# Kernel tuning notes

Hardware: AMD Instinct MI355X
Metric: run time of the kernel (lower is better)

The kernel has to match this reference:

```python
import jax, jax.numpy as jnp
import numpy as np

NUM_ENTITIES = 64
PAD, BOS, EOS = 0, 1, 2
B, S = 512, 512


def setup_inputs() -> dict:
    key = jax.random.key(0)
    k1, k2, k3 = jax.random.split(key, 3)
    emissions = jax.random.normal(k1, (B, S, NUM_ENTITIES), dtype=jnp.float32)
    entities = jax.random.randint(k2, (B, S), 0, NUM_ENTITIES)
    mask = jnp.ones((B, S), dtype=bool)
    # transitions param, initialized as in _init_transitions
    t = jax.random.uniform(k3, (NUM_ENTITIES, NUM_ENTITIES), jnp.float32, -0.1, 0.1)
    t = t.at[:, BOS].set(-10000.0)
    t = t.at[EOS, :].set(-10000.0)
    t = t.at[PAD, :].set(-10000.0)
    t = t.at[:, PAD].set(-10000.0)
    t = t.at[PAD, PAD].set(0.0)
    t = t.at[PAD, EOS].set(0.0)
    return {"emissions": emissions, "transitions": t, "entities": entities, "mask": mask}


def _crf_nll(emissions, transitions, entities, mask):
    mf = mask.astype(emissions.dtype)  # [B,S]
    # ---- gold path score (vectorized over time) ----
    first = entities[:, 0]
    last_idx = jnp.sum(mask.astype(jnp.int32), axis=1) - 1  # [B]
    last = jnp.take_along_axis(entities, last_idx[:, None], axis=1)[:, 0]
    e = jnp.take_along_axis(emissions, entities[:, :, None], axis=2)[:, :, 0]  # [B,S]
    t = transitions[entities[:, :-1], entities[:, 1:]]  # [B,S-1]
    score = (transitions[BOS, first] + e[:, 0]
             + jnp.sum((e[:, 1:] + t) * mf[:, 1:], axis=1)
             + transitions[last, EOS])  # [B]
    # ---- log partition via scan over time ----
    alpha0 = transitions[BOS][None, :] + emissions[:, 0]  # [B,E]

    def step(alpha, xs):
        em_t, m_t = xs  # [B,E], [B] bool
        # scores[b, prev, cur] = alpha[b,prev] + T[prev,cur] + em[b,cur]
        scores = alpha[:, :, None] + transitions[None, :, :] + em_t[:, None, :]
        new_alpha = jax.nn.logsumexp(scores, axis=1)  # [B,E]
        alpha = jnp.where(m_t[:, None], new_alpha, alpha)
        return alpha, None

    alpha, _ = jax.lax.scan(step, alpha0,
                            (jnp.swapaxes(emissions[:, 1:], 0, 1), mask[:, 1:].T))
    log_z = jax.nn.logsumexp(alpha + transitions[:, EOS][None, :], axis=1)  # [B]
    return -jnp.mean(score - log_z)


def reference(emissions, transitions, entities, mask):
    return _crf_nll(emissions, transitions, entities, mask)
```

## Files before the change

### kernel.cpp

```cpp
#include <hip/hip_runtime.h>

#define NE 64
#define BB 512
#define SS 512
#define TMID 256
#define NBWD (SS - 1 - TMID)
#define NCHAIN 32
#define BOS_S 1
#define EOS_S 2
#define LN2 0.69314718055994531f
#define DR 8

typedef float f32x4 __attribute__((ext_vector_type(4)));
typedef int   i32x4 __attribute__((ext_vector_type(4)));
typedef short bf16x8 __attribute__((ext_vector_type(8)));

#define WG_SCOPE __HIP_MEMORY_SCOPE_WORKGROUP

__device__ __forceinline__ float wave_sum(float v) {
#pragma unroll
    for (int off = 32; off > 0; off >>= 1)
        v += __shfl_xor(v, off, 64);
    return v;
}

__device__ __forceinline__ unsigned pack2(float lo, float hi) {
    return __builtin_amdgcn_perm(__float_as_uint(hi), __float_as_uint(lo), 0x07060302u);
}

__device__ __forceinline__ unsigned short bf16_rne(float f) {
    unsigned u = __float_as_uint(f);
    return (unsigned short)((u + 0x7fffu + ((u >> 16) & 1u)) >> 16);
}

template <bool FWD>
__device__ __forceinline__ void producer_loop(const float* embase, float (*ring)[1024],
                                              int* ready, int* cons, int p, int lane,
                                              int tmax) {
    int t = 1 + p;
    f32x4 b0[4], b1[4];
    if (t <= tmax) {
        const float* r = embase + (size_t)(FWD ? t : (SS - t)) * NE;
#pragma unroll
        for (int m = 0; m < 4; ++m) b0[m] = *(const f32x4*)(r + 16 * m);
    }
    if (t + 3 <= tmax) {
        const float* r = embase + (size_t)(FWD ? (t + 3) : (SS - t - 3)) * NE;
#pragma unroll
        for (int m = 0; m < 4; ++m) b1[m] = *(const f32x4*)(r + 16 * m);
    }
    while (t <= tmax) {
        int tn2 = t + 6;
        f32x4 nb[4];
        if (tn2 <= tmax) {
            const float* r = embase + (size_t)(FWD ? tn2 : (SS - tn2)) * NE;
#pragma unroll
            for (int m = 0; m < 4; ++m) nb[m] = *(const f32x4*)(r + 16 * m);
        }
        while (__hip_atomic_load(cons, __ATOMIC_ACQUIRE, WG_SCOPE) < t - DR)
            __builtin_amdgcn_s_sleep(1);
        int slot = t & (DR - 1);
        f32x4* dst = (f32x4*)ring[slot];
#pragma unroll
        for (int m = 0; m < 4; ++m) {
            f32x4 w;
#pragma unroll
            for (int r2 = 0; r2 < 4; ++r2) w[r2] = __expf(b0[m][r2]);
            dst[m * 64 + lane] = w;
        }
        __hip_atomic_store(&ready[slot], t, __ATOMIC_RELEASE, WG_SCOPE);
#pragma unroll
        for (int m = 0; m < 4; ++m) { b0[m] = b1[m]; b1[m] = nb[m]; }
        t += 3;
    }
}

__global__ __launch_bounds__(512, 1) void crf_fused(const float* __restrict__ em,
                                                    const float* __restrict__ T,
                                                    const int* __restrict__ ent,
                                                    float* __restrict__ out_mean) {
    const int lane = threadIdx.x & 63;
    const int wv = threadIdx.x >> 6;

    if (blockIdx.x >= NCHAIN) {
        const int b = (blockIdx.x - NCHAIN) * 8 + wv;
        const float* emb = em + (size_t)b * SS * NE;
        const int* entb = ent + b * SS;
        float sc = 0.f;
        for (int t = lane; t < SS; t += 64) {
            int et = entb[t];
            sc += emb[t * NE + et];
            sc += (t == 0) ? T[BOS_S * NE + et] : T[entb[t - 1] * NE + et];
            if (t == SS - 1) sc += T[et * NE + EOS_S];
        }
        sc = wave_sum(sc);
        if (lane == 0) atomicAdd(out_mean, -sc * (1.0f / (float)BB));
        return;
    }

    __shared__ float ringf[DR][1024];
    __shared__ float ringb[DR][1024];
    __shared__ int readyf[DR], readyb[DR];
    __shared__ int consf, consb;
    __shared__ float wbuf[1024];
    __shared__ int shiftb_s;
    __shared__ int doneb;

    if (threadIdx.x < DR) { readyf[threadIdx.x] = 0; readyb[threadIdx.x] = 0; }
    if (threadIdx.x == 0) { consf = 0; consb = 0; doneb = 0; }
    __syncthreads();

    const int g = blockIdx.x;
    const int n = lane & 15;
    const int q = lane >> 4;

    if (wv >= 2) {
        const float* embase = em + ((size_t)(g * 16 + n) * SS) * NE + 4 * q;
        if (wv <= 4)
            producer_loop<true>(embase, ringf, readyf, &consf, wv - 2, lane, TMID);
        else
            producer_loop<false>(embase, ringb, readyb, &consb, wv - 5, lane, NBWD);
        return;
    }

#define PIPE_FLAGS(RING, READY, T_, GNXT, DO_LOAD)                               \
    do {                                                                         \
        int _fprev = fnext;                                                      \
        fnext = __hip_atomic_load(&READY[((T_) + 2) & (DR - 1)],                 \
                                  __ATOMIC_RELAXED, WG_SCOPE);                   \
        if (DO_LOAD) {                                                           \
            if (__builtin_expect(_fprev != (T_) + 1, 0)) {                       \
                while (__hip_atomic_load(&READY[((T_) + 1) & (DR - 1)],          \
                                         __ATOMIC_ACQUIRE, WG_SCOPE) != (T_) + 1) {} \
            }                                                                    \
            const f32x4* _src = (const f32x4*)RING[((T_) + 1) & (DR - 1)];       \
            GNXT[0] = _src[0 * 64 + lane];                                       \
            GNXT[1] = _src[1 * 64 + lane];                                       \
            GNXT[2] = _src[2 * 64 + lane];                                       \
            GNXT[3] = _src[3 * 64 + lane];                                       \
        }                                                                        \
    } while (0)

#define CONS_STORE(CONS, T_)                                                     \
    do {                                                                         \
        asm volatile("" ::: "memory");      \
        if ((((T_) & 1) == 0) && lane == 0)                                      \
            __hip_atomic_store(&CONS, (T_), __ATOMIC_RELAXED, WG_SCOPE);         \
    } while (0)


#define STEP_F(T_, GCUR, GNXT, DO_LOAD, DO_NORM)                                 \
    do {                                                                         \
        PIPE_FLAGS(ringf, readyf, T_, GNXT, DO_LOAD);                            \
        float ds[16];                                                            \
        if (DO_NORM) {                                                           \
            unsigned u3 = (unsigned)__builtin_amdgcn_readlane(__float_as_int(d[3]), 0); \
            int kk = (int)((u3 >> 23) & 255u) - 127;                             \
            shift += kk;                                                         \
            float scale = __uint_as_float((unsigned)(127 - kk) << 23);           \
            _Pragma("unroll") for (int v = 0; v < 16; ++v) ds[v] = d[v] * scale; \
        } else {                                                                 \
            _Pragma("unroll") for (int v = 0; v < 16; ++v) ds[v] = d[v];         \
        }                                                                        \
        i32x4 bi0, bi1;                                                          \
        bi0[0] = (int)pack2(ds[0], ds[1]);   bi0[1] = (int)pack2(ds[2], ds[3]);  \
        bi0[2] = (int)pack2(ds[4], ds[5]);   bi0[3] = (int)pack2(ds[6], ds[7]);  \
        bi1[0] = (int)pack2(ds[8], ds[9]);   bi1[1] = (int)pack2(ds[10], ds[11]);\
        bi1[2] = (int)pack2(ds[12], ds[13]); bi1[3] = (int)pack2(ds[14], ds[15]);\
        bf16x8 B0 = __builtin_bit_cast(bf16x8, bi0);                             \
        bf16x8 B1 = __builtin_bit_cast(bf16x8, bi1);                             \
        _Pragma("unroll") for (int tm = 0; tm < 4; ++tm) {                       \
            f32x4 z4 = {0.f, 0.f, 0.f, 0.f};                                     \
            f32x4 acc0 = __builtin_amdgcn_mfma_f32_16x16x32_bf16(A[tm][0], B0, z4, 0, 0, 0); \
            f32x4 acc1 = __builtin_amdgcn_mfma_f32_16x16x32_bf16(A[tm][1], B1, z4, 0, 0, 0); \
            _Pragma("unroll") for (int r = 0; r < 4; ++r)                        \
                d[4 * tm + r] = (acc0[r] + acc1[r]) * GCUR[tm][r];               \
        }                                                                        \
        CONS_STORE(consf, T_);                                                   \
    } while (0)

#define STEP_B(T_, GCUR, GNXT, DO_LOAD, DO_NORM)                                 \
    do {                                                                         \
        PIPE_FLAGS(ringb, readyb, T_, GNXT, DO_LOAD);                            \
        float ds[16];                                                            \
        if (DO_NORM) {                                                           \
            unsigned u3 = (unsigned)__builtin_amdgcn_readlane(__float_as_int(d[3]), 0); \
            int kk = (int)((u3 >> 23) & 255u) - 127;                             \
            shift += kk;                                                         \
            float scale = __uint_as_float((unsigned)(127 - kk) << 23);           \
            _Pragma("unroll") for (int v = 0; v < 16; ++v)                       \
                ds[v] = (d[v] * GCUR[v >> 2][v & 3]) * scale;                    \
        } else {                                                                 \
            _Pragma("unroll") for (int v = 0; v < 16; ++v)                       \
                ds[v] = d[v] * GCUR[v >> 2][v & 3];                              \
        }                                                                        \
        i32x4 bi0, bi1;                                                          \
        bi0[0] = (int)pack2(ds[0], ds[1]);   bi0[1] = (int)pack2(ds[2], ds[3]);  \
        bi0[2] = (int)pack2(ds[4], ds[5]);   bi0[3] = (int)pack2(ds[6], ds[7]);  \
        bi1[0] = (int)pack2(ds[8], ds[9]);   bi1[1] = (int)pack2(ds[10], ds[11]);\
        bi1[2] = (int)pack2(ds[12], ds[13]); bi1[3] = (int)pack2(ds[14], ds[15]);\
        bf16x8 B0 = __builtin_bit_cast(bf16x8, bi0);                             \
        bf16x8 B1 = __builtin_bit_cast(bf16x8, bi1);                             \
        _Pragma("unroll") for (int tm = 0; tm < 4; ++tm) {                       \
            f32x4 z4 = {0.f, 0.f, 0.f, 0.f};                                     \
            f32x4 acc0 = __builtin_amdgcn_mfma_f32_16x16x32_bf16(A[tm][0], B0, z4, 0, 0, 0); \
            f32x4 acc1 = __builtin_amdgcn_mfma_f32_16x16x32_bf16(A[tm][1], B1, z4, 0, 0, 0); \
            _Pragma("unroll") for (int r = 0; r < 4; ++r)                        \
                d[4 * tm + r] = acc0[r] + acc1[r];                               \
        }                                                                        \
        CONS_STORE(consb, T_);                                                   \
    } while (0)

    if (wv == 0) {
        __builtin_amdgcn_s_setprio(1);
        const int b = g * 16 + n;

        bf16x8 A[4][2];
#pragma unroll
        for (int tm = 0; tm < 4; ++tm)
#pragma unroll
            for (int kt = 0; kt < 2; ++kt) {
                i32x4 w;
#pragma unroll
                for (int pp = 0; pp < 4; ++pp) {
                    int j0 = 2 * pp, j1 = 2 * pp + 1;
                    int s0 = 16 * (2 * kt + (j0 >> 2)) + 4 * q + (j0 & 3);
                    int s1 = 16 * (2 * kt + (j1 >> 2)) + 4 * q + (j1 & 3);
                    int m = 16 * tm + n;
                    unsigned lo = bf16_rne(__expf(T[s0 * NE + m]));
                    unsigned hi = bf16_rne(__expf(T[s1 * NE + m]));
                    w[pp] = (int)(lo | (hi << 16));
                }
                A[tm][kt] = __builtin_bit_cast(bf16x8, w);
            }

        const float* pe = em + (size_t)b * SS * NE + 4 * q;
        float d[16];
        {
            f32x4 e0[4];
#pragma unroll
            for (int m = 0; m < 4; ++m) e0[m] = *(const f32x4*)(pe + 16 * m);
#pragma unroll
            for (int v = 0; v < 16; ++v) {
                int s = 16 * (v >> 2) + 4 * q + (v & 3);
                d[v] = __expf(T[BOS_S * NE + s] + e0[v >> 2][v & 3]);
            }
        }

        int shift = 0;
        f32x4 GA[4], GB[4];
        while (__hip_atomic_load(&readyf[1], __ATOMIC_ACQUIRE, WG_SCOPE) != 1) {}
        {
            const f32x4* _src = (const f32x4*)ringf[1];
            GA[0] = _src[0 * 64 + lane]; GA[1] = _src[1 * 64 + lane];
            GA[2] = _src[2 * 64 + lane]; GA[3] = _src[3 * 64 + lane];
        }
        int fnext = __hip_atomic_load(&readyf[2], __ATOMIC_RELAXED, WG_SCOPE);

        int t = 1;
        for (; t + 4 <= TMID; t += 4) {
            STEP_F(t,     GA, GB, 1, 1);
            STEP_F(t + 1, GB, GA, 1, 0);
            STEP_F(t + 2, GA, GB, 1, 0);
            STEP_F(t + 3, GB, GA, 1, 0);
        }
        STEP_F(t,     GA, GB, 1, 1);
        STEP_F(t + 1, GB, GA, 1, 0);
        STEP_F(t + 2, GA, GB, 1, 0);
        STEP_F(t + 3, GB, GA, 0, 0);

        while (__hip_atomic_load(&doneb, __ATOMIC_ACQUIRE, WG_SCOPE) == 0) {}
        int sb = shiftb_s;
        const float* wp = wbuf + n * 64 + q * 16;
        float partial = 0.f;
#pragma unroll
        for (int v = 0; v < 16; ++v) partial = fmaf(d[v], wp[v], partial);
        partial += __shfl_xor(partial, 16, 64);
        partial += __shfl_xor(partial, 32, 64);

        float log_z = (float)(shift + sb) * LN2 + __logf(partial);
        float val = (lane < 16) ? log_z * (1.0f / (float)BB) : 0.f;
        val = wave_sum(val);
        if (lane == 0) atomicAdd(out_mean, val);
        return;
    }

    {
        __builtin_amdgcn_s_setprio(1);
        bf16x8 A[4][2];
#pragma unroll
        for (int tm = 0; tm < 4; ++tm)
#pragma unroll
            for (int kt = 0; kt < 2; ++kt) {
                i32x4 w;
#pragma unroll
                for (int pp = 0; pp < 4; ++pp) {
                    int j0 = 2 * pp, j1 = 2 * pp + 1;
                    int s0 = 16 * (2 * kt + (j0 >> 2)) + 4 * q + (j0 & 3);
                    int s1 = 16 * (2 * kt + (j1 >> 2)) + 4 * q + (j1 & 3);
                    int m = 16 * tm + n;
                    unsigned lo = bf16_rne(__expf(T[m * NE + s0]));
                    unsigned hi = bf16_rne(__expf(T[m * NE + s1]));
                    w[pp] = (int)(lo | (hi << 16));
                }
                A[tm][kt] = __builtin_bit_cast(bf16x8, w);
            }

        float d[16];
#pragma unroll
        for (int v = 0; v < 16; ++v) {
            int s = 16 * (v >> 2) + 4 * q + (v & 3);
            d[v] = __expf(T[s * NE + EOS_S]);
        }

        int shift = 0;
        f32x4 GA[4], GB[4];
        while (__hip_atomic_load(&readyb[1], __ATOMIC_ACQUIRE, WG_SCOPE) != 1) {}
        {
            const f32x4* _src = (const f32x4*)ringb[1];
            GA[0] = _src[0 * 64 + lane]; GA[1] = _src[1 * 64 + lane];
            GA[2] = _src[2 * 64 + lane]; GA[3] = _src[3 * 64 + lane];
        }
        int fnext = __hip_atomic_load(&readyb[2], __ATOMIC_RELAXED, WG_SCOPE);

        int vt = 1;
        for (; vt + 4 <= NBWD; vt += 4) {
            STEP_B(vt,     GA, GB, 1, 1);
            STEP_B(vt + 1, GB, GA, 1, 0);
            STEP_B(vt + 2, GA, GB, 1, 0);
            STEP_B(vt + 3, GB, GA, 1, 0);
        }
        STEP_B(vt,     GA, GB, 1, 1);
        STEP_B(vt + 1, GB, GA, 1, 0);
        STEP_B(vt + 2, GA, GB, 0, 0);

        float* wp = wbuf + n * 64 + q * 16;
#pragma unroll
        for (int v = 0; v < 16; ++v) wp[v] = d[v];
        if (lane == 0) {
            shiftb_s = shift;
            __hip_atomic_store(&doneb, 1, __ATOMIC_RELEASE, WG_SCOPE);
        }
        return;
    }
#undef STEP_F
#undef STEP_B
#undef PIPE_FLAGS
#undef CONS_STORE
}

extern "C" void kernel_launch(void* const* d_in, const int* in_sizes, int n_in,
                              void* d_out, int out_size, void* d_ws, size_t ws_size,
                              hipStream_t stream) {
    const float* emissions   = (const float*)d_in[0];
    const float* transitions = (const float*)d_in[1];
    const int*   entities    = (const int*)d_in[2];

    hipMemsetAsync(d_out, 0, sizeof(float), stream);
    crf_fused<<<NCHAIN + BB / 8, 512, 0, stream>>>(emissions, transitions, entities,
                                                   (float*)d_out);
}
```

Baseline: 81.06 us.

## Use one producer wave per direction with 4-deep register prefetch, 256-thread blocks

Each direction's emission producer is cut from three interleaved waves to a single wave. That wave unrolls its loop by four, keeps four timesteps of prefetched emission rows in registers, and has the step bound fixed at compile time. The block shrinks from 512 to 256 threads, the gold-score blocks handle four sequences each, and the grid grows to match. The setprio calls on the consumer waves are also removed. The aim is less wave contention and scheduling overhead on the CU running each chain. The risk is that one producer wave cannot keep up with the consumer's exp-and-store rate, which would stall the recurrence.

```diff
diff --git a/kernel.cpp b/kernel.cpp
--- a/kernel.cpp
+++ b/kernel.cpp
@@ -33,49 +33,57 @@
     return (unsigned short)((u + 0x7fffu + ((u >> 16) & 1u)) >> 16);
 }
 
-template <bool FWD>
+template <bool FWD, int TMAX>
 __device__ __forceinline__ void producer_loop(const float* embase, float (*ring)[1024],
-                                              int* ready, int* cons, int p, int lane,
-                                              int tmax) {
-    int t = 1 + p;
-    f32x4 b0[4], b1[4];
-    if (t <= tmax) {
-        const float* r = embase + (size_t)(FWD ? t : (SS - t)) * NE;
-#pragma unroll
-        for (int m = 0; m < 4; ++m) b0[m] = *(const f32x4*)(r + 16 * m);
-    }
-    if (t + 3 <= tmax) {
-        const float* r = embase + (size_t)(FWD ? (t + 3) : (SS - t - 3)) * NE;
-#pragma unroll
-        for (int m = 0; m < 4; ++m) b1[m] = *(const f32x4*)(r + 16 * m);
-    }
-    while (t <= tmax) {
-        int tn2 = t + 6;
-        f32x4 nb[4];
-        if (tn2 <= tmax) {
-            const float* r = embase + (size_t)(FWD ? tn2 : (SS - tn2)) * NE;
-#pragma unroll
-            for (int m = 0; m < 4; ++m) nb[m] = *(const f32x4*)(r + 16 * m);
-        }
-        while (__hip_atomic_load(cons, __ATOMIC_ACQUIRE, WG_SCOPE) < t - DR)
-            __builtin_amdgcn_s_sleep(1);
-        int slot = t & (DR - 1);
-        f32x4* dst = (f32x4*)ring[slot];
-#pragma unroll
-        for (int m = 0; m < 4; ++m) {
-            f32x4 w;
-#pragma unroll
-            for (int r2 = 0; r2 < 4; ++r2) w[r2] = __expf(b0[m][r2]);
-            dst[m * 64 + lane] = w;
-        }
-        __hip_atomic_store(&ready[slot], t, __ATOMIC_RELEASE, WG_SCOPE);
-#pragma unroll
-        for (int m = 0; m < 4; ++m) { b0[m] = b1[m]; b1[m] = nb[m]; }
-        t += 3;
-    }
-}
-
-__global__ __launch_bounds__(512, 1) void crf_fused(const float* __restrict__ em,
+                                              int* ready, int* cons, int lane) {
+    f32x4 b[4][4];
+#pragma unroll
+    for (int j = 0; j < 4; ++j) {
+        int t = 1 + j;
+        if (t <= TMAX) {
+            const float* r = embase + (size_t)(FWD ? t : (SS - t)) * NE;
+#pragma unroll
+            for (int m = 0; m < 4; ++m) b[j][m] = *(const f32x4*)(r + 16 * m);
+        }
+    }
+#define PROD_PHASE(J, T_)                                                        \
+    do {                                                                         \
+        f32x4 nb[4];                                                             \
+        const bool _pf = (T_) + 4 <= TMAX;                                       \
+        if (_pf) {                                                               \
+            const float* r = embase + (size_t)(FWD ? ((T_) + 4) : (SS - (T_) - 4)) * NE; \
+            _Pragma("unroll") for (int m = 0; m < 4; ++m)                        \
+                nb[m] = *(const f32x4*)(r + 16 * m);                             \
+        }                                                                        \
+        while (__hip_atomic_load(cons, __ATOMIC_ACQUIRE, WG_SCOPE) < (T_) - DR)  \
+            __builtin_amdgcn_s_sleep(1);                                         \
+        f32x4* dst = (f32x4*)ring[(T_) & (DR - 1)];                              \
+        _Pragma("unroll") for (int m = 0; m < 4; ++m) {                          \
+            f32x4 w;                                                             \
+            _Pragma("unroll") for (int r2 = 0; r2 < 4; ++r2)                     \
+                w[r2] = __expf(b[J][m][r2]);                                     \
+            dst[m * 64 + lane] = w;                                              \
+        }                                                                        \
+        __hip_atomic_store(&ready[(T_) & (DR - 1)], (T_), __ATOMIC_RELEASE, WG_SCOPE); \
+        if (_pf) { _Pragma("unroll") for (int m = 0; m < 4; ++m) b[J][m] = nb[m]; } \
+    } while (0)
+
+    int tb = 1;
+    for (; tb + 3 <= TMAX; tb += 4) {
+        PROD_PHASE(0, tb);
+        PROD_PHASE(1, tb + 1);
+        PROD_PHASE(2, tb + 2);
+        PROD_PHASE(3, tb + 3);
+    }
+    if (TMAX % 4 == 3) {
+        PROD_PHASE(0, tb);
+        PROD_PHASE(1, tb + 1);
+        PROD_PHASE(2, tb + 2);
+    }
+#undef PROD_PHASE
+}
+
+__global__ __launch_bounds__(256, 1) void crf_fused(const float* __restrict__ em,
                                                     const float* __restrict__ T,
                                                     const int* __restrict__ ent,
                                                     float* __restrict__ out_mean) {
@@ -83,7 +91,7 @@
     const int wv = threadIdx.x >> 6;
 
     if (blockIdx.x >= NCHAIN) {
-        const int b = (blockIdx.x - NCHAIN) * 8 + wv;
+        const int b = (blockIdx.x - NCHAIN) * 4 + wv;
         const float* emb = em + (size_t)b * SS * NE;
         const int* entb = ent + b * SS;
         float sc = 0.f;
@@ -116,10 +124,10 @@
 
     if (wv >= 2) {
         const float* embase = em + ((size_t)(g * 16 + n) * SS) * NE + 4 * q;
-        if (wv <= 4)
-            producer_loop<true>(embase, ringf, readyf, &consf, wv - 2, lane, TMID);
+        if (wv == 2)
+            producer_loop<true, TMID>(embase, ringf, readyf, &consf, lane);
         else
-            producer_loop<false>(embase, ringb, readyb, &consb, wv - 5, lane, NBWD);
+            producer_loop<false, NBWD>(embase, ringb, readyb, &consb, lane);
         return;
     }
 
@@ -212,7 +220,6 @@
     } while (0)
 
     if (wv == 0) {
-        __builtin_amdgcn_s_setprio(1);
         const int b = g * 16 + n;
 
         bf16x8 A[4][2];
@@ -286,7 +293,6 @@
     }
 
     {
-        __builtin_amdgcn_s_setprio(1);
         bf16x8 A[4][2];
 #pragma unroll
         for (int tm = 0; tm < 4; ++tm)
@@ -357,6 +363,6 @@
     const int*   entities    = (const int*)d_in[2];
 
     hipMemsetAsync(d_out, 0, sizeof(float), stream);
-    crf_fused<<<NCHAIN + BB / 8, 512, 0, stream>>>(emissions, transitions, entities,
+    crf_fused<<<NCHAIN + BB / 4, 256, 0, stream>>>(emissions, transitions, entities,
                                                    (float*)d_out);
 }
```

After: 123.4 us. +52.3%, slower.
